# Kernel tuning notes

Hardware: AMD Instinct MI355X
Metric: run time of the kernel (lower is better)

The kernel has to match this reference:

```python
import jax, jax.numpy as jnp
import numpy as np
from jax import lax

WINDOW = 3  # box-filter window (matches init kwarg)


def setup_inputs() -> dict:
    key = jax.random.key(0)
    y_pred = jax.random.normal(key, (1, 3, 192, 192, 192), dtype=jnp.float32)
    return {"y_pred": y_pred}


def _box_filter(x, win):
    pad = win // 2
    kernel = jnp.ones((3, 1, win, win, win), dtype=x.dtype) / (win ** 3)
    return lax.conv_general_dilated(
        x, kernel,
        window_strides=(1, 1, 1),
        padding=[(pad, pad)] * 3,
        dimension_numbers=("NCDHW", "OIDHW", "NCDHW"),
        feature_group_count=3,
    )


def reference(y_pred):
    base = y_pred[:, :, :-1, :-1, :-1]
    dy = jnp.abs(y_pred[:, :, 1:, :-1, :-1] - base)
    dx = jnp.abs(y_pred[:, :, :-1, 1:, :-1] - base)
    dz = jnp.abs(y_pred[:, :, :-1, :-1, 1:] - base)

    fdx = _box_filter(dx, WINDOW)  # [B,3,D-1,H-1,W-1]
    fdy = _box_filter(dy, WINDOW)
    fdz = _box_filter(dz, WINDOW)

    dxdx, dxdy, dxdz = fdx[:, 1:2], fdy[:, 1:2], fdz[:, 1:2]
    dydx, dydy, dydz = fdx[:, 0:1], fdy[:, 0:1], fdz[:, 0:1]
    dzdx, dzdy, dzdz = fdx[:, 2:3], fdy[:, 2:3], fdz[:, 2:3]

    det_1 = (dxdx + 1) * ((dydy + 1) * (dzdz + 1) - dydz * dzdy)
    det_2 = -dxdy * (dydx * (dzdz + 1) - dydz * dzdx)
    det_3 = dxdz * (dydx * dzdy - (dydy + 1) * dzdx)
    J = det_1 + det_2 + det_3
    return jnp.squeeze(J)  # [D-1, H-1, W-1] for B=1
```

## Files before the change

kernel.cpp:

```cpp
#include <hip/hip_runtime.h>

#define NSZ   192
#define NSZ2  (NSZ*NSZ)
#define NSZ3  (NSZ*NSZ*NSZ)
#define N1    191
#define TW    64
#define TH    8
#define TD    16
#define LROWS 11
#define PADW  72
#define ROWF4 18
#define SLOTF4 594
#define SLOTF  (SLOTF4*4)
#define NTHREADS 256

__device__ __forceinline__ void gload_lds16(const float* g, float* l) {
    __builtin_amdgcn_global_load_lds((const __attribute__((address_space(1))) void*)g,
                                     (__attribute__((address_space(3))) void*)l, 16, 0, 0);
}

__device__ __forceinline__ void ld3f2(float* d, const float* p) {
    *(float2*)&d[0] = *(const float2*)&p[0];
    *(float2*)&d[2] = *(const float2*)&p[2];
    *(float2*)&d[4] = *(const float2*)&p[4];
}

__device__ __forceinline__ void stage(const float* __restrict__ y, float* slot,
                                      int s, const int* goff, int tid) {
    const float* src = y + (size_t)s * NSZ2;
    gload_lds16(src + goff[0], slot + (size_t)tid * 4);
    gload_lds16(src + goff[1], slot + (size_t)(tid + 256) * 4);
    if (tid < SLOTF4 - 512)
        gload_lds16(src + goff[2], slot + (size_t)(tid + 512) * 4);
}

#define ROWC(A0, A1, B, rv, FIRST)                                               \
    {   float dh0=A1[1]-A0[1], dh1=A1[2]-A0[2], dh2=A1[3]-A0[3], dh3=A1[4]-A0[4];\
        float dd0=B[1]-A0[1],  dd1=B[2]-A0[2],  dd2=B[3]-A0[3],  dd3=B[4]-A0[4]; \
        float dw0=A0[2]-A0[1], dw1=A0[3]-A0[2], dw2=A0[4]-A0[3], dw3=A0[5]-A0[4];\
        float eH = fmaf(colv[2], fabsf(dh2), colv[1]*fabsf(dh1));                \
        float tH0 = fmaf(colv[0], fabsf(dh0), eH);                               \
        float tH1 = fmaf(colv[3], fabsf(dh3), eH);                               \
        float eD = fmaf(colv[2], fabsf(dd2), colv[1]*fabsf(dd1));                \
        float tD0 = fmaf(colv[0], fabsf(dd0), eD);                               \
        float tD1 = fmaf(colv[3], fabsf(dd3), eD);                               \
        float eW = fmaf(colv[2], fabsf(dw2), colv[1]*fabsf(dw1));                \
        float tW0 = fmaf(colv[0], fabsf(dw0), eW);                               \
        float tW1 = fmaf(colv[3], fabsf(dw3), eW);                               \
        if (FIRST) { aH0=tH0; aH1=tH1; aD0=rv*tD0; aD1=rv*tD1;                   \
                     aW0=rv*tW0; aW1=rv*tW1; }                                   \
        else { aH0+=tH0; aH1+=tH1; aD0=fmaf(rv,tD0,aD0); aD1=fmaf(rv,tD1,aD1);   \
               aW0=fmaf(rv,tW0,aW0); aW1=fmaf(rv,tW1,aW1); } }

__global__ __launch_bounds__(NTHREADS, 2)
void jac_kernel(const float* __restrict__ y, float* __restrict__ out) {
    __shared__ __align__(16) float lds[3 * SLOTF];

    const int tx = threadIdx.x;
    const int ty = threadIdx.y;
    const int tid = ty * 32 + tx;
    const int w0 = blockIdx.x * TW;
    const int h0 = blockIdx.y * TH;
    const int d0 = blockIdx.z * TD;
    const int j  = h0 + ty;
    const int k0 = w0 + 2 * tx;

    float colv[4], rowv[3];
    #pragma unroll
    for (int p = 0; p < 4; ++p) { int gk = k0 - 1 + p; colv[p] = (gk >= 0 && gk < N1) ? 1.f : 0.f; }
    #pragma unroll
    for (int r = 0; r < 3; ++r) { int gr = j - 1 + r; rowv[r] = (gr >= 0 && gr < N1) ? 1.f : 0.f; }

    int goff[3];
    #pragma unroll
    for (int k = 0; k < 3; ++k) {
        int e4 = tid + k * 256; if (e4 > SLOTF4 - 1) e4 = SLOTF4 - 1;
        int rowi = e4 / ROWF4, m = e4 - rowi * ROWF4;
        int ch = rowi / LROWS, rr = rowi - ch * LROWS;
        int gr = h0 - 1 + rr; gr = gr < 0 ? 0 : (gr > N1 ? N1 : gr);
        int c4 = w0 - 4 + 4 * m; c4 = c4 < 0 ? 0 : (c4 > NSZ - 4 ? NSZ - 4 : c4);
        goff[k] = ch * NSZ3 + gr * NSZ + c4;
    }

    float a1[18], bb[18];
    #pragma unroll
    for (int t = 0; t < 18; ++t) { a1[t] = 0.f; bb[t] = 0.f; }

    if (d0 >= 1) stage(y, lds + ((d0 + 2) % 3) * SLOTF, d0 - 1, goff, tid);
    stage(y, lds + (d0 % 3) * SLOTF, d0, goff, tid);
    __syncthreads();

    const int rowoff = ty * PADW + 2 * tx + 2;

    float c[3][3][6];
    {
        const float* base = lds + (((d0 >= 1) ? (d0 - 1) : d0) % 3) * SLOTF + rowoff;
        #pragma unroll
        for (int ch = 0; ch < 3; ++ch) {
            const float* p = base + ch * (LROWS * PADW);
            ld3f2(c[ch][0], p);
            ld3f2(c[ch][1], p + PADW);
            ld3f2(c[ch][2], p + 2 * PADW);
        }
    }

    float* pa = lds + ((d0 + 2) % 3) * SLOTF;
    float* pb = lds + (d0 % 3) * SLOTF;
    float* pc = lds + ((d0 + 1) % 3) * SLOTF;

    #pragma unroll 3
    for (int ii = 0; ii < TD + 2; ++ii) {
        const int i = d0 - 1 + ii;

        if (ii <= TD && i + 2 <= N1) stage(y, pc, i + 2, goff, tid);

        float f[18];
        if (i >= 0 && i < N1) {
            #pragma unroll
            for (int ch = 0; ch < 3; ++ch) {
                const float* bA = pa + ch * (LROWS * PADW) + rowoff;
                const float* bB = pb + ch * (LROWS * PADW) + rowoff;
                float a3[6];
                ld3f2(a3, bA + 3 * PADW);
                float b0[6], b1[6], b2[6];
                ld3f2(b0, bB); ld3f2(b1, bB + PADW); ld3f2(b2, bB + 2 * PADW);
                float aH0, aH1, aD0, aD1, aW0, aW1;
                ROWC(c[ch][0], c[ch][1], b0, rowv[0], 1)
                ROWC(c[ch][1], c[ch][2], b1, rowv[1], 0)
                ROWC(c[ch][2], a3,       b2, rowv[2], 0)
                const int gi = ch * 6;
                f[gi+0]=bb[gi+0]+aH0; bb[gi+0]=a1[gi+0]+aH0; a1[gi+0]=aH0;
                f[gi+1]=bb[gi+1]+aH1; bb[gi+1]=a1[gi+1]+aH1; a1[gi+1]=aH1;
                f[gi+2]=bb[gi+2]+aD0; bb[gi+2]=a1[gi+2]+aD0; a1[gi+2]=aD0;
                f[gi+3]=bb[gi+3]+aD1; bb[gi+3]=a1[gi+3]+aD1; a1[gi+3]=aD1;
                f[gi+4]=bb[gi+4]+aW0; bb[gi+4]=a1[gi+4]+aW0; a1[gi+4]=aW0;
                f[gi+5]=bb[gi+5]+aW1; bb[gi+5]=a1[gi+5]+aW1; a1[gi+5]=aW1;
                #pragma unroll
                for (int p = 0; p < 6; ++p) {
                    c[ch][0][p] = b0[p]; c[ch][1][p] = b1[p]; c[ch][2][p] = b2[p];
                }
            }
        } else {
            #pragma unroll
            for (int t = 0; t < 18; ++t) { f[t] = bb[t]; bb[t] = a1[t]; a1[t] = 0.f; }
        }

        const int d = i - 1;
        if (ii >= 2 && d < N1 && j < N1) {
            const float K = 27.f, KS = 1.f / 19683.f;
            #pragma unroll
            for (int q = 0; q < 2; ++q) {
                if (k0 + q < N1) {
                    float ayx = f[0+q],  ayy = f[2+q],  ayz = f[4+q];
                    float axx = f[6+q],  axy = f[8+q],  axz = f[10+q];
                    float azx = f[12+q], azy = f[14+q], azz = f[16+q];
                    float ayyK = ayy + K, azzK = azz + K, axxK = axx + K;
                    float t = fmaf(-ayz, azy, ayyK * azzK);
                    float v = fmaf(-ayz, azx, ayx * azzK);
                    float w = fmaf(-ayyK, azx, ayx * azy);
                    float R = axxK * t;
                    R = fmaf(-axy, v, R);
                    R = fmaf(axz, w, R);
                    out[(d * N1 + j) * N1 + (k0 + q)] = R * KS;
                }
            }
        }

        __syncthreads();
        float* tp = pa; pa = pb; pb = pc; pc = tp;
    }
}

extern "C" void kernel_launch(void* const* d_in, const int* in_sizes, int n_in,
                              void* d_out, int out_size, void* d_ws, size_t ws_size,
                              hipStream_t stream) {
    const float* y = (const float*)d_in[0];
    float* out = (float*)d_out;
    dim3 grid(3, 24, 12);
    dim3 block(32, 8, 1);
    jac_kernel<<<grid, block, 0, stream>>>(y, out);
}
```

Measured before the change: 65.22 us.

## Deepen LDS staging to four slots and wait on older loads only

Moves from a 3-slot to a 4-slot LDS ring, so each depth slice is prefetched two iterations ahead. The full __syncthreads is replaced by a manual s_waitcnt vmcnt(3) plus s_barrier, letting the newest async global->LDS loads stay in flight across the barrier. It also drops the tail guard on the third staging load, since slots are now padded to 3072 floats. The cost is more LDS per block (48KB vs about 28KB), which may limit occupancy. Correctness now depends on the hand-written vmcnt accounting matching the compiler's issued loads.

```diff
diff --git a/kernel.cpp b/kernel.cpp
--- a/kernel.cpp
+++ b/kernel.cpp
@@ -11,7 +11,7 @@
 #define PADW  72
 #define ROWF4 18
 #define SLOTF4 594
-#define SLOTF  (SLOTF4*4)
+#define SLOTP  3072
 #define NTHREADS 256
 
 __device__ __forceinline__ void gload_lds16(const float* g, float* l) {
@@ -30,8 +30,7 @@
     const float* src = y + (size_t)s * NSZ2;
     gload_lds16(src + goff[0], slot + (size_t)tid * 4);
     gload_lds16(src + goff[1], slot + (size_t)(tid + 256) * 4);
-    if (tid < SLOTF4 - 512)
-        gload_lds16(src + goff[2], slot + (size_t)(tid + 512) * 4);
+    gload_lds16(src + goff[2], slot + (size_t)(tid + 512) * 4);
 }
 
 #define ROWC(A0, A1, B, rv, FIRST)                                               \
@@ -54,7 +53,7 @@
 
 __global__ __launch_bounds__(NTHREADS, 2)
 void jac_kernel(const float* __restrict__ y, float* __restrict__ out) {
-    __shared__ __align__(16) float lds[3 * SLOTF];
+    __shared__ __align__(16) float lds[4 * SLOTP];
 
     const int tx = threadIdx.x;
     const int ty = threadIdx.y;
@@ -86,15 +85,21 @@
     #pragma unroll
     for (int t = 0; t < 18; ++t) { a1[t] = 0.f; bb[t] = 0.f; }
 
-    if (d0 >= 1) stage(y, lds + ((d0 + 2) % 3) * SLOTF, d0 - 1, goff, tid);
-    stage(y, lds + (d0 % 3) * SLOTF, d0, goff, tid);
+    float* p0 = lds;
+    float* p1 = lds + SLOTP;
+    float* p2 = lds + 2 * SLOTP;
+    float* p3 = lds + 3 * SLOTP;
+
+    if (d0 >= 1) stage(y, p0, d0 - 1, goff, tid);
+    stage(y, p1, d0, goff, tid);
+    stage(y, p2, d0 + 1, goff, tid);
     __syncthreads();
 
     const int rowoff = ty * PADW + 2 * tx + 2;
 
     float c[3][3][6];
     {
-        const float* base = lds + (((d0 >= 1) ? (d0 - 1) : d0) % 3) * SLOTF + rowoff;
+        const float* base = (d0 >= 1 ? p0 : p1) + rowoff;
         #pragma unroll
         for (int ch = 0; ch < 3; ++ch) {
             const float* p = base + ch * (LROWS * PADW);
@@ -104,22 +109,18 @@
         }
     }
 
-    float* pa = lds + ((d0 + 2) % 3) * SLOTF;
-    float* pb = lds + (d0 % 3) * SLOTF;
-    float* pc = lds + ((d0 + 1) % 3) * SLOTF;
-
-    #pragma unroll 3
     for (int ii = 0; ii < TD + 2; ++ii) {
         const int i = d0 - 1 + ii;
+        const bool stage_now = (ii <= TD - 1) && (i + 3 <= N1);
 
-        if (ii <= TD && i + 2 <= N1) stage(y, pc, i + 2, goff, tid);
+        if (stage_now) stage(y, p3, i + 3, goff, tid);
 
         float f[18];
         if (i >= 0 && i < N1) {
             #pragma unroll
             for (int ch = 0; ch < 3; ++ch) {
-                const float* bA = pa + ch * (LROWS * PADW) + rowoff;
-                const float* bB = pb + ch * (LROWS * PADW) + rowoff;
+                const float* bA = p0 + ch * (LROWS * PADW) + rowoff;
+                const float* bB = p1 + ch * (LROWS * PADW) + rowoff;
                 float a3[6];
                 ld3f2(a3, bA + 3 * PADW);
                 float b0[6], b1[6], b2[6];
@@ -166,8 +167,11 @@
             }
         }
 
-        __syncthreads();
-        float* tp = pa; pa = pb; pb = pc; pc = tp;
+        if (stage_now) { asm volatile("s_waitcnt vmcnt(3)" ::: "memory"); }
+        else           { asm volatile("s_waitcnt vmcnt(0)" ::: "memory"); }
+        __builtin_amdgcn_s_barrier();
+
+        float* tp = p0; p0 = p1; p1 = p2; p2 = p3; p3 = tp;
     }
 }
 
```

Measured after the change: 70.26 us. 7.7% more time.
